# Kernel optimization log

Measured on AMD Instinct MI355X. Metric: run time of the kernel, lower is better.

The kernel has to match this reference:

```python
import jax, jax.numpy as jnp
import numpy as np

B, T, D_IN, D_FEAT, D_LAT = 256, 512, 128, 256, 512

def setup_inputs() -> dict:
    key = jax.random.key(0)
    ks = jax.random.split(key, 6)
    s = lambda fan_in: 1.0 / np.sqrt(fan_in)
    return {
        "x": jax.random.normal(ks[0], (B, T, D_IN), dtype=jnp.float32),
        "W_enc": jax.random.normal(ks[1], (D_IN, D_FEAT), dtype=jnp.float32) * s(D_IN),
        "b_enc": jnp.zeros((D_FEAT,), dtype=jnp.float32),
        "W_x": jax.random.normal(ks[2], (D_FEAT, 4 * D_LAT), dtype=jnp.float32) * s(D_FEAT),
        "W_h": jax.random.normal(ks[3], (D_LAT, 4 * D_LAT), dtype=jnp.float32) * s(D_LAT),
        "b_lstm": jnp.zeros((4 * D_LAT,), dtype=jnp.float32),
        "W_dec": jax.random.normal(ks[4], (D_LAT, 1), dtype=jnp.float32) * s(D_LAT),
        "b_dec": jnp.zeros((1,), dtype=jnp.float32),
    }

def reference(x, W_enc, b_enc, W_x, W_h, b_lstm, W_dec, b_dec):
    # Dense encoder with tanh: [B,T,D_IN] -> [B,T,D_FEAT]
    enc = jnp.tanh(jnp.einsum("bti,if->btf", x, W_enc) + b_enc)
    d = W_h.shape[0]
    # Precompute input-to-gate projection for all steps (hoisted out of loop)
    xz = jnp.einsum("btf,fg->btg", enc, W_x) + b_lstm  # [B,T,4d]
    xz_t = jnp.swapaxes(xz, 0, 1)  # [T,B,4d] for scan

    def step(carry, xz_step):
        h, c = carry
        z = xz_step + h @ W_h  # [B,4d]
        i, f, g, o = jnp.split(z, 4, axis=-1)  # Keras gate order: i,f,c,o
        i = jax.nn.sigmoid(i)
        f = jax.nn.sigmoid(f)
        g = jnp.tanh(g)
        o = jax.nn.sigmoid(o)
        c_new = f * c + i * g
        h_new = o * jnp.tanh(c_new)
        return (h_new, c_new), None

    h0 = jnp.zeros((x.shape[0], d), dtype=x.dtype)
    c0 = jnp.zeros((x.shape[0], d), dtype=x.dtype)
    (h_last, _), _ = jax.lax.scan(step, (h0, c0), xz_t)
    # Decoder on last hidden state: [B,d] -> [B,1]
    return h_last @ W_dec + b_dec
```

## Files before the change

### kernel.cpp

```cpp
#include <hip/hip_runtime.h>

#define BATCH 256
#define TLEN  512
#define DIN   128
#define DFEAT 256
#define DLAT  512
#define G4    2048
#define KCAT  768

typedef __bf16 bf16x8 __attribute__((ext_vector_type(8)));
typedef float f32x4 __attribute__((ext_vector_type(4)));

typedef __attribute__((address_space(1))) const unsigned int glb_u32;
typedef __attribute__((address_space(3))) unsigned int lds_u32;

#define WCAT_OFF   0u
#define WENC_OFF   3145728u
#define ENC_OFF    3211264u
#define H_OFF      70320128u
#define FLAG_OFF   70844416u

__device__ __forceinline__ float sigf(float x)  { return 1.0f / (1.0f + __expf(-x)); }
__device__ __forceinline__ float tanhfast(float x){ return 2.0f / (1.0f + __expf(-2.0f * x)) - 1.0f; }
__device__ __forceinline__ unsigned short bfb(float f) {
    __bf16 b = (__bf16)f;
    return __builtin_bit_cast(unsigned short, b);
}

__global__ __launch_bounds__(256) void wprep_kernel(const float* __restrict__ Wx,
                                                    const float* __restrict__ Wh,
                                                    const float* __restrict__ Wenc,
                                                    __bf16* __restrict__ wcat,
                                                    __bf16* __restrict__ wencf) {
    int cid = blockIdx.x * 256 + threadIdx.x;
    float v[8];
    __bf16* dst;
    if (cid < 196608) {
        int widx = cid / 12288;
        int r1 = cid % 12288;
        int nn = r1 / 1536;
        int r2 = r1 % 1536;
        int ks = r2 >> 6, l = r2 & 63;
        int col = (nn >> 1) * 512 + widx * 32 + (nn & 1) * 16 + (l & 15);
        int kc = ks * 32 + (l >> 4) * 8;
#pragma unroll
        for (int j = 0; j < 8; ++j) {
            int kk = kc + j;
            v[j] = (kk < DFEAT) ? Wx[kk * G4 + col] : Wh[(kk - DFEAT) * G4 + col];
        }
        dst = wcat + (size_t)cid * 8;
    } else {
        int c2 = cid - 196608;
        int ntg = c2 >> 8;
        int r = c2 & 255;
        int ks = r >> 6, l = r & 63;
        int col = ntg * 16 + (l & 15);
        int kc = ks * 32 + (l >> 4) * 8;
#pragma unroll
        for (int j = 0; j < 8; ++j) v[j] = Wenc[(kc + j) * DFEAT + col];
        dst = wencf + (size_t)c2 * 8;
    }
    bf16x8 o;
#pragma unroll
    for (int j = 0; j < 8; ++j) o[j] = (__bf16)v[j];
    *reinterpret_cast<bf16x8*>(dst) = o;
}

__global__ __launch_bounds__(256) void enc_kernel(const float* __restrict__ x,
                                                  const float* __restrict__ benc,
                                                  const __bf16* __restrict__ wencf,
                                                  __bf16* __restrict__ enc) {
    __shared__ uint4 afrag4[1024];
    __bf16* afrag = reinterpret_cast<__bf16*>(afrag4);
    int tid = threadIdx.x;
    int lane = tid & 63, w = tid >> 6;
    int rid0 = blockIdx.x * 64;
    int ntg0 = blockIdx.y * 4;

    bf16x8 wr[4][4];
#pragma unroll
    for (int n = 0; n < 4; ++n)
#pragma unroll
        for (int ks = 0; ks < 4; ++ks)
            wr[n][ks] = *reinterpret_cast<const bf16x8*>(
                wencf + (size_t)(((ntg0 + n) * 4 + ks) * 64 + lane) * 8);
    float bias[4];
#pragma unroll
    for (int n = 0; n < 4; ++n) bias[n] = benc[(ntg0 + n) * 16 + (lane & 15)];

#pragma unroll
    for (int i = 0; i < 4; ++i) {
        int c = tid + 256 * i;
        int row = c >> 4, k8 = c & 15;
        const float* src = x + (size_t)(rid0 + row) * DIN + k8 * 8;
        float4 f0 = *reinterpret_cast<const float4*>(src);
        float4 f1 = *reinterpret_cast<const float4*>(src + 4);
        bf16x8 o;
        o[0] = (__bf16)f0.x; o[1] = (__bf16)f0.y; o[2] = (__bf16)f0.z; o[3] = (__bf16)f0.w;
        o[4] = (__bf16)f1.x; o[5] = (__bf16)f1.y; o[6] = (__bf16)f1.z; o[7] = (__bf16)f1.w;
        int l = (k8 & 3) * 16 + (row & 15);
        int a16 = ((row >> 4) * 4 + (k8 >> 2)) * 64 + l;
        *reinterpret_cast<bf16x8*>(afrag + (size_t)a16 * 8) = o;
    }
    __syncthreads();

    int m = w;
    f32x4 acc[4];
#pragma unroll
    for (int n = 0; n < 4; ++n) acc[n] = (f32x4){bias[n], bias[n], bias[n], bias[n]};
#pragma unroll
    for (int ks = 0; ks < 4; ++ks) {
        bf16x8 a = *reinterpret_cast<const bf16x8*>(afrag + (size_t)((m * 4 + ks) * 64 + lane) * 8);
#pragma unroll
        for (int n = 0; n < 4; ++n)
            acc[n] = __builtin_amdgcn_mfma_f32_16x16x32_bf16(a, wr[n][ks], acc[n], 0, 0, 0);
    }
#pragma unroll
    for (int n = 0; n < 4; ++n) {
        int colg = (ntg0 + n) * 16 + (lane & 15);
#pragma unroll
        for (int q = 0; q < 4; ++q) {
            int rid = rid0 + m * 16 + (lane >> 4) * 4 + q;
            int bb = rid >> 9, tt = rid & 511;
            float th = tanhfast(acc[n][q]);
            enc[(size_t)(tt * BATCH + bb) * DFEAT + colg] = (__bf16)th;
        }
    }
}

__global__ __launch_bounds__(256, 1) void lstm_kernel(const __bf16* __restrict__ enc,
                                                      const __bf16* __restrict__ wcat,
                                                      const float* __restrict__ blstm,
                                                      __bf16* __restrict__ hbuf,
                                                      unsigned int* __restrict__ flags) {
    extern __shared__ char smem[];
    __bf16* afrag = reinterpret_cast<__bf16*>(smem);
    float* zbuf = reinterpret_cast<float*>(smem + 24576);

    const int tid = threadIdx.x;
    const int lane = tid & 63, np = tid >> 6;
    const int grp = blockIdx.x & 15, widx = blockIdx.x >> 4;
    const int b0 = grp * 16;

    bf16x8 wreg[2][24];
#pragma unroll
    for (int nt2 = 0; nt2 < 2; ++nt2)
#pragma unroll
        for (int ks = 0; ks < 24; ++ks)
            wreg[nt2][ks] = *reinterpret_cast<const bf16x8*>(
                wcat + (size_t)((((widx * 8 + np * 2 + nt2) * 24) + ks) * 64 + lane) * 8);
    const float bias0 = blstm[np * 512 + widx * 32 + (lane & 15)];
    const float bias1 = blstm[np * 512 + widx * 32 + 16 + (lane & 15)];

    const int row = tid & 15;
    const int kq = (tid >> 6) * 32 + ((tid >> 4) & 3) * 8;
    const __bf16* encp = enc + (size_t)(b0 + row) * DFEAT + kq;
    const __bf16* hpA = hbuf + (size_t)(b0 + row) * DLAT + kq;
    const __bf16* hpB = hpA + (size_t)BATCH * DLAT;
    __bf16* enc_lds = afrag + tid * 8;
    __bf16* h_lds = afrag + (512 + tid) * 8;
    const int cell = 2 * tid;
    const int crow = cell >> 5, ccol = cell & 31;
    unsigned* hdA = reinterpret_cast<unsigned*>(
        hbuf + (size_t)(b0 + crow) * DLAT + widx * 32 + ccol);
    unsigned* hdB = reinterpret_cast<unsigned*>(
        hbuf + (size_t)BATCH * DLAT + (size_t)(b0 + crow) * DLAT + widx * 32 + ccol);
    const unsigned* pollp = &flags[(grp * 16 + (lane >> 2)) * 16 + (lane & 3)];
    unsigned* myflag = &flags[(grp * 16 + widx) * 16 + np];
    const float* zg = zbuf + crow * 32 + ccol;
    float* zst = zbuf + np * 512 + ((lane >> 4) * 4) * 32 + (lane & 15);
    const __bf16* abase = afrag + lane * 8;

    float c0 = 0.f, c1 = 0.f;

    __builtin_amdgcn_global_load_lds((glb_u32*)encp, (lds_u32*)enc_lds, 16, 0, 0);
    __builtin_amdgcn_global_load_lds((glb_u32*)(encp + 128), (lds_u32*)(enc_lds + 2048), 16, 0, 0);
    encp += (size_t)BATCH * DFEAT;
    __syncthreads();

#pragma unroll 1
    for (int t = 0; t < TLEN; ++t) {
        f32x4 acc0 = (f32x4){bias0, bias0, bias0, bias0};
        f32x4 acc1 = (f32x4){bias1, bias1, bias1, bias1};
#pragma unroll
        for (int ks = 0; ks < 8; ++ks) {
            bf16x8 a = *reinterpret_cast<const bf16x8*>(abase + ks * 512);
            acc0 = __builtin_amdgcn_mfma_f32_16x16x32_bf16(a, wreg[0][ks], acc0, 0, 0, 0);
            acc1 = __builtin_amdgcn_mfma_f32_16x16x32_bf16(a, wreg[1][ks], acc1, 0, 0, 0);
        }

        if (t > 0) {
            unsigned v;
            do {
                v = __hip_atomic_load(pollp, __ATOMIC_RELAXED, __HIP_MEMORY_SCOPE_AGENT);
            } while (!__all((int)(v >= (unsigned)t)));

            const __bf16* hp = (t & 1) ? hpB : hpA;
            uint4 d0, d1, d2, d3;
            asm volatile(
                "global_load_dwordx4 %0, %4, off sc1\n\t"
                "global_load_dwordx4 %1, %4, off offset:256 sc1\n\t"
                "global_load_dwordx4 %2, %4, off offset:512 sc1\n\t"
                "global_load_dwordx4 %3, %4, off offset:768 sc1\n\t"
                "s_waitcnt vmcnt(0)"
                : "=&v"(d0), "=&v"(d1), "=&v"(d2), "=&v"(d3)
                : "v"(hp) : "memory");
            *reinterpret_cast<uint4*>(h_lds) = d0;
            *reinterpret_cast<uint4*>(h_lds + 2048) = d1;
            *reinterpret_cast<uint4*>(h_lds + 4096) = d2;
            *reinterpret_cast<uint4*>(h_lds + 6144) = d3;
            __syncthreads();

#pragma unroll
            for (int ks = 8; ks < 24; ++ks) {
                bf16x8 a = *reinterpret_cast<const bf16x8*>(abase + ks * 512);
                acc0 = __builtin_amdgcn_mfma_f32_16x16x32_bf16(a, wreg[0][ks], acc0, 0, 0, 0);
                acc1 = __builtin_amdgcn_mfma_f32_16x16x32_bf16(a, wreg[1][ks], acc1, 0, 0, 0);
            }
        }

#pragma unroll
        for (int q = 0; q < 4; ++q) {
            zst[q * 32] = acc0[q];
            zst[q * 32 + 16] = acc1[q];
        }
        __syncthreads();

        float2 zi = *reinterpret_cast<const float2*>(zg);
        float2 zf = *reinterpret_cast<const float2*>(zg + 512);
        float2 zgt = *reinterpret_cast<const float2*>(zg + 1024);
        float2 zo = *reinterpret_cast<const float2*>(zg + 1536);
        float i0 = sigf(zi.x), f0 = sigf(zf.x), g0 = tanhfast(zgt.x), o0 = sigf(zo.x);
        c0 = f0 * c0 + i0 * g0;
        float h0 = o0 * tanhfast(c0);
        float i1 = sigf(zi.y), f1 = sigf(zf.y), g1 = tanhfast(zgt.y), o1 = sigf(zo.y);
        c1 = f1 * c1 + i1 * g1;
        float h1 = o1 * tanhfast(c1);

        unsigned hpk = (unsigned)bfb(h0) | ((unsigned)bfb(h1) << 16);
        __hip_atomic_store(((t & 1) ? hdA : hdB), hpk, __ATOMIC_RELAXED,
                           __HIP_MEMORY_SCOPE_AGENT);

        asm volatile("s_waitcnt vmcnt(0)" ::: "memory");
        if (lane == 0)
            __hip_atomic_store(myflag, (unsigned)(t + 1), __ATOMIC_RELAXED,
                               __HIP_MEMORY_SCOPE_AGENT);

        if (t + 1 < TLEN) {
            __builtin_amdgcn_global_load_lds((glb_u32*)encp, (lds_u32*)enc_lds, 16, 0, 0);
            __builtin_amdgcn_global_load_lds((glb_u32*)(encp + 128),
                                             (lds_u32*)(enc_lds + 2048), 16, 0, 0);
            encp += (size_t)BATCH * DFEAT;
        }
        __syncthreads();
    }
}

__global__ __launch_bounds__(64) void dec_kernel(const __bf16* __restrict__ hbuf,
                                                 const float* __restrict__ wdec,
                                                 const float* __restrict__ bdec,
                                                 float* __restrict__ out) {
    int b = blockIdx.x, lane = threadIdx.x;
    uint4 d = *reinterpret_cast<const uint4*>(hbuf + (size_t)b * DLAT + lane * 8);
    const __bf16* hv = reinterpret_cast<const __bf16*>(&d);
    float4 w0 = *reinterpret_cast<const float4*>(wdec + lane * 8);
    float4 w1 = *reinterpret_cast<const float4*>(wdec + lane * 8 + 4);
    float s = (float)hv[0] * w0.x + (float)hv[1] * w0.y + (float)hv[2] * w0.z +
              (float)hv[3] * w0.w + (float)hv[4] * w1.x + (float)hv[5] * w1.y +
              (float)hv[6] * w1.z + (float)hv[7] * w1.w;
#pragma unroll
    for (int off = 32; off; off >>= 1) s += __shfl_xor(s, off);
    if (lane == 0) out[b] = s + bdec[0];
}

extern "C" void kernel_launch(void* const* d_in, const int* in_sizes, int n_in,
                              void* d_out, int out_size, void* d_ws, size_t ws_size,
                              hipStream_t stream) {
    (void)in_sizes; (void)n_in; (void)out_size; (void)ws_size;
    const float* x     = (const float*)d_in[0];
    const float* Wenc  = (const float*)d_in[1];
    const float* benc  = (const float*)d_in[2];
    const float* Wx    = (const float*)d_in[3];
    const float* Wh    = (const float*)d_in[4];
    const float* blstm = (const float*)d_in[5];
    const float* Wdec  = (const float*)d_in[6];
    const float* bdec  = (const float*)d_in[7];

    char* ws = (char*)d_ws;
    __bf16* wcat  = (__bf16*)(ws + WCAT_OFF);
    __bf16* wencf = (__bf16*)(ws + WENC_OFF);
    __bf16* enc   = (__bf16*)(ws + ENC_OFF);
    __bf16* hbuf  = (__bf16*)(ws + H_OFF);
    unsigned int* flags = (unsigned int*)(ws + FLAG_OFF);

    (void)hipMemsetAsync(ws + FLAG_OFF, 0, 16384, stream);

    wprep_kernel<<<784, 256, 0, stream>>>(Wx, Wh, Wenc, wcat, wencf);
    enc_kernel<<<dim3(2048, 4), 256, 0, stream>>>(x, benc, wencf, enc);

    (void)hipFuncSetAttribute(reinterpret_cast<const void*>(lstm_kernel),
                              hipFuncAttributeMaxDynamicSharedMemorySize, 90112);
    lstm_kernel<<<256, 256, 90112, stream>>>(enc, wcat, blstm, hbuf, flags);

    dec_kernel<<<256, 64, 0, stream>>>(hbuf, Wdec, bdec, (float*)d_out);
}
```

Baseline: 1.539 ms.

## Tag hidden-state words with step counter to replace flag polling

Each bf16 hidden value is now stored in a 32-bit word with a 16-bit step tag in the low half, so consumers poll the data itself until every tag matches the current step. This removes the separate flag array, the vmcnt wait before the flag store, and one round-trip of flag polling per step. The LSTM kernel also converts Wx/Wh to bf16 fragments directly from fp32 inside its prologue, which drops the weight-prep work for those matrices. In exchange the h exchange traffic doubles, and spinning on many data lines with s_sleep may add latency or memory contention.

```diff
diff --git a/kernel.cpp b/kernel.cpp
--- a/kernel.cpp
+++ b/kernel.cpp
@@ -14,11 +14,9 @@
 typedef __attribute__((address_space(1))) const unsigned int glb_u32;
 typedef __attribute__((address_space(3))) unsigned int lds_u32;
 
-#define WCAT_OFF   0u
-#define WENC_OFF   3145728u
-#define ENC_OFF    3211264u
-#define H_OFF      70320128u
-#define FLAG_OFF   70844416u
+#define WENC_OFF   0u
+#define ENC_OFF    65536u
+#define H_OFF      67174400u
 
 __device__ __forceinline__ float sigf(float x)  { return 1.0f / (1.0f + __expf(-x)); }
 __device__ __forceinline__ float tanhfast(float x){ return 2.0f / (1.0f + __expf(-2.0f * x)) - 1.0f; }
@@ -26,44 +24,22 @@
     __bf16 b = (__bf16)f;
     return __builtin_bit_cast(unsigned short, b);
 }
-
-__global__ __launch_bounds__(256) void wprep_kernel(const float* __restrict__ Wx,
-                                                    const float* __restrict__ Wh,
-                                                    const float* __restrict__ Wenc,
-                                                    __bf16* __restrict__ wcat,
+__device__ __forceinline__ float bfu(unsigned w) {
+    return (float)__builtin_bit_cast(__bf16, (unsigned short)(w >> 16));
+}
+
+__global__ __launch_bounds__(256) void wprep_kernel(const float* __restrict__ Wenc,
                                                     __bf16* __restrict__ wencf) {
-    int cid = blockIdx.x * 256 + threadIdx.x;
-    float v[8];
-    __bf16* dst;
-    if (cid < 196608) {
-        int widx = cid / 12288;
-        int r1 = cid % 12288;
-        int nn = r1 / 1536;
-        int r2 = r1 % 1536;
-        int ks = r2 >> 6, l = r2 & 63;
-        int col = (nn >> 1) * 512 + widx * 32 + (nn & 1) * 16 + (l & 15);
-        int kc = ks * 32 + (l >> 4) * 8;
-#pragma unroll
-        for (int j = 0; j < 8; ++j) {
-            int kk = kc + j;
-            v[j] = (kk < DFEAT) ? Wx[kk * G4 + col] : Wh[(kk - DFEAT) * G4 + col];
-        }
-        dst = wcat + (size_t)cid * 8;
-    } else {
-        int c2 = cid - 196608;
-        int ntg = c2 >> 8;
-        int r = c2 & 255;
-        int ks = r >> 6, l = r & 63;
-        int col = ntg * 16 + (l & 15);
-        int kc = ks * 32 + (l >> 4) * 8;
-#pragma unroll
-        for (int j = 0; j < 8; ++j) v[j] = Wenc[(kc + j) * DFEAT + col];
-        dst = wencf + (size_t)c2 * 8;
-    }
+    int c2 = blockIdx.x * 256 + threadIdx.x;
+    int ntg = c2 >> 8;
+    int r = c2 & 255;
+    int ks = r >> 6, l = r & 63;
+    int col = ntg * 16 + (l & 15);
+    int kc = ks * 32 + (l >> 4) * 8;
     bf16x8 o;
 #pragma unroll
-    for (int j = 0; j < 8; ++j) o[j] = (__bf16)v[j];
-    *reinterpret_cast<bf16x8*>(dst) = o;
+    for (int j = 0; j < 8; ++j) o[j] = (__bf16)Wenc[(kc + j) * DFEAT + col];
+    *reinterpret_cast<bf16x8*>(wencf + (size_t)c2 * 8) = o;
 }
 
 __global__ __launch_bounds__(256) void enc_kernel(const float* __restrict__ x,
@@ -129,10 +105,10 @@
 }
 
 __global__ __launch_bounds__(256, 1) void lstm_kernel(const __bf16* __restrict__ enc,
-                                                      const __bf16* __restrict__ wcat,
+                                                      const float* __restrict__ Wx,
+                                                      const float* __restrict__ Wh,
                                                       const float* __restrict__ blstm,
-                                                      __bf16* __restrict__ hbuf,
-                                                      unsigned int* __restrict__ flags) {
+                                                      unsigned* __restrict__ hbuf) {
     extern __shared__ char smem[];
     __bf16* afrag = reinterpret_cast<__bf16*>(smem);
     float* zbuf = reinterpret_cast<float*>(smem + 24576);
@@ -144,29 +120,38 @@
 
     bf16x8 wreg[2][24];
 #pragma unroll
-    for (int nt2 = 0; nt2 < 2; ++nt2)
-#pragma unroll
-        for (int ks = 0; ks < 24; ++ks)
-            wreg[nt2][ks] = *reinterpret_cast<const bf16x8*>(
-                wcat + (size_t)((((widx * 8 + np * 2 + nt2) * 24) + ks) * 64 + lane) * 8);
+    for (int nt2 = 0; nt2 < 2; ++nt2) {
+        const int col = np * 512 + widx * 32 + nt2 * 16 + (lane & 15);
+#pragma unroll
+        for (int ks = 0; ks < 24; ++ks) {
+            const int kb = ks * 32 + (lane >> 4) * 8;
+            bf16x8 f;
+#pragma unroll
+            for (int j = 0; j < 8; ++j) {
+                int kk = kb + j;
+                float w = (kk < DFEAT) ? Wx[(size_t)kk * G4 + col]
+                                       : Wh[(size_t)(kk - DFEAT) * G4 + col];
+                f[j] = (__bf16)w;
+            }
+            wreg[nt2][ks] = f;
+        }
+    }
     const float bias0 = blstm[np * 512 + widx * 32 + (lane & 15)];
     const float bias1 = blstm[np * 512 + widx * 32 + 16 + (lane & 15)];
 
     const int row = tid & 15;
     const int kq = (tid >> 6) * 32 + ((tid >> 4) & 3) * 8;
     const __bf16* encp = enc + (size_t)(b0 + row) * DFEAT + kq;
-    const __bf16* hpA = hbuf + (size_t)(b0 + row) * DLAT + kq;
-    const __bf16* hpB = hpA + (size_t)BATCH * DLAT;
+    const unsigned* hpA = hbuf + (size_t)(b0 + row) * DLAT + kq;
+    const unsigned* hpB = hpA + (size_t)BATCH * DLAT;
     __bf16* enc_lds = afrag + tid * 8;
     __bf16* h_lds = afrag + (512 + tid) * 8;
     const int cell = 2 * tid;
     const int crow = cell >> 5, ccol = cell & 31;
-    unsigned* hdA = reinterpret_cast<unsigned*>(
+    unsigned long long* hd0 = reinterpret_cast<unsigned long long*>(
         hbuf + (size_t)(b0 + crow) * DLAT + widx * 32 + ccol);
-    unsigned* hdB = reinterpret_cast<unsigned*>(
+    unsigned long long* hd1 = reinterpret_cast<unsigned long long*>(
         hbuf + (size_t)BATCH * DLAT + (size_t)(b0 + crow) * DLAT + widx * 32 + ccol);
-    const unsigned* pollp = &flags[(grp * 16 + (lane >> 2)) * 16 + (lane & 3)];
-    unsigned* myflag = &flags[(grp * 16 + widx) * 16 + np];
     const float* zg = zbuf + crow * 32 + ccol;
     float* zst = zbuf + np * 512 + ((lane >> 4) * 4) * 32 + (lane & 15);
     const __bf16* abase = afrag + lane * 8;
@@ -190,25 +175,30 @@
         }
 
         if (t > 0) {
-            unsigned v;
-            do {
-                v = __hip_atomic_load(pollp, __ATOMIC_RELAXED, __HIP_MEMORY_SCOPE_AGENT);
-            } while (!__all((int)(v >= (unsigned)t)));
-
-            const __bf16* hp = (t & 1) ? hpB : hpA;
-            uint4 d0, d1, d2, d3;
-            asm volatile(
-                "global_load_dwordx4 %0, %4, off sc1\n\t"
-                "global_load_dwordx4 %1, %4, off offset:256 sc1\n\t"
-                "global_load_dwordx4 %2, %4, off offset:512 sc1\n\t"
-                "global_load_dwordx4 %3, %4, off offset:768 sc1\n\t"
-                "s_waitcnt vmcnt(0)"
-                : "=&v"(d0), "=&v"(d1), "=&v"(d2), "=&v"(d3)
-                : "v"(hp) : "memory");
-            *reinterpret_cast<uint4*>(h_lds) = d0;
-            *reinterpret_cast<uint4*>(h_lds + 2048) = d1;
-            *reinterpret_cast<uint4*>(h_lds + 4096) = d2;
-            *reinterpret_cast<uint4*>(h_lds + 6144) = d3;
+            const unsigned tlo = (unsigned)t & 0xffffu;
+            const unsigned* hp = (t & 1) ? hpB : hpA;
+#pragma unroll
+            for (int ii = 0; ii < 4; ++ii) {
+                const unsigned* p = hp + ii * 128;
+                uint4 a, b;
+                for (;;) {
+                    asm volatile(
+                        "global_load_dwordx4 %0, %2, off sc1\n\t"
+                        "global_load_dwordx4 %1, %2, off offset:16 sc1\n\t"
+                        "s_waitcnt vmcnt(0)"
+                        : "=&v"(a), "=&v"(b) : "v"(p) : "memory");
+                    unsigned m = ((a.x ^ tlo) | (a.y ^ tlo) | (a.z ^ tlo) | (a.w ^ tlo) |
+                                  (b.x ^ tlo) | (b.y ^ tlo) | (b.z ^ tlo) | (b.w ^ tlo)) & 0xffffu;
+                    if (m == 0) break;
+                    __builtin_amdgcn_s_sleep(1);
+                }
+                uint4 o;
+                o.x = (a.x >> 16) | (a.y & 0xffff0000u);
+                o.y = (a.z >> 16) | (a.w & 0xffff0000u);
+                o.z = (b.x >> 16) | (b.y & 0xffff0000u);
+                o.w = (b.z >> 16) | (b.w & 0xffff0000u);
+                *reinterpret_cast<uint4*>(h_lds + ii * 2048) = o;
+            }
             __syncthreads();
 
 #pragma unroll
@@ -237,14 +227,12 @@
         c1 = f1 * c1 + i1 * g1;
         float h1 = o1 * tanhfast(c1);
 
-        unsigned hpk = (unsigned)bfb(h0) | ((unsigned)bfb(h1) << 16);
-        __hip_atomic_store(((t & 1) ? hdA : hdB), hpk, __ATOMIC_RELAXED,
+        const unsigned tago = (unsigned)(t + 1) & 0xffffu;
+        unsigned w0 = ((unsigned)bfb(h0) << 16) | tago;
+        unsigned w1 = ((unsigned)bfb(h1) << 16) | tago;
+        unsigned long long pk = (unsigned long long)w0 | ((unsigned long long)w1 << 32);
+        __hip_atomic_store(((t & 1) ? hd0 : hd1), pk, __ATOMIC_RELAXED,
                            __HIP_MEMORY_SCOPE_AGENT);
-
-        asm volatile("s_waitcnt vmcnt(0)" ::: "memory");
-        if (lane == 0)
-            __hip_atomic_store(myflag, (unsigned)(t + 1), __ATOMIC_RELAXED,
-                               __HIP_MEMORY_SCOPE_AGENT);
 
         if (t + 1 < TLEN) {
             __builtin_amdgcn_global_load_lds((glb_u32*)encp, (lds_u32*)enc_lds, 16, 0, 0);
@@ -256,18 +244,18 @@
     }
 }
 
-__global__ __launch_bounds__(64) void dec_kernel(const __bf16* __restrict__ hbuf,
+__global__ __launch_bounds__(64) void dec_kernel(const unsigned* __restrict__ hbuf,
                                                  const float* __restrict__ wdec,
                                                  const float* __restrict__ bdec,
                                                  float* __restrict__ out) {
     int b = blockIdx.x, lane = threadIdx.x;
-    uint4 d = *reinterpret_cast<const uint4*>(hbuf + (size_t)b * DLAT + lane * 8);
-    const __bf16* hv = reinterpret_cast<const __bf16*>(&d);
+    const unsigned* hrow = hbuf + (size_t)b * DLAT + lane * 8;
+    uint4 a = *reinterpret_cast<const uint4*>(hrow);
+    uint4 c = *reinterpret_cast<const uint4*>(hrow + 4);
     float4 w0 = *reinterpret_cast<const float4*>(wdec + lane * 8);
     float4 w1 = *reinterpret_cast<const float4*>(wdec + lane * 8 + 4);
-    float s = (float)hv[0] * w0.x + (float)hv[1] * w0.y + (float)hv[2] * w0.z +
-              (float)hv[3] * w0.w + (float)hv[4] * w1.x + (float)hv[5] * w1.y +
-              (float)hv[6] * w1.z + (float)hv[7] * w1.w;
+    float s = bfu(a.x) * w0.x + bfu(a.y) * w0.y + bfu(a.z) * w0.z + bfu(a.w) * w0.w +
+              bfu(c.x) * w1.x + bfu(c.y) * w1.y + bfu(c.z) * w1.z + bfu(c.w) * w1.w;
 #pragma unroll
     for (int off = 32; off; off >>= 1) s += __shfl_xor(s, off);
     if (lane == 0) out[b] = s + bdec[0];
@@ -287,20 +275,18 @@
     const float* bdec  = (const float*)d_in[7];
 
     char* ws = (char*)d_ws;
-    __bf16* wcat  = (__bf16*)(ws + WCAT_OFF);
     __bf16* wencf = (__bf16*)(ws + WENC_OFF);
     __bf16* enc   = (__bf16*)(ws + ENC_OFF);
-    __bf16* hbuf  = (__bf16*)(ws + H_OFF);
-    unsigned int* flags = (unsigned int*)(ws + FLAG_OFF);
-
-    (void)hipMemsetAsync(ws + FLAG_OFF, 0, 16384, stream);
-
-    wprep_kernel<<<784, 256, 0, stream>>>(Wx, Wh, Wenc, wcat, wencf);
+    unsigned* hbuf = (unsigned*)(ws + H_OFF);
+
+    (void)hipMemsetAsync(ws + H_OFF, 0, 1048576, stream);
+
+    wprep_kernel<<<16, 256, 0, stream>>>(Wenc, wencf);
     enc_kernel<<<dim3(2048, 4), 256, 0, stream>>>(x, benc, wencf, enc);
 
     (void)hipFuncSetAttribute(reinterpret_cast<const void*>(lstm_kernel),
                               hipFuncAttributeMaxDynamicSharedMemorySize, 90112);
-    lstm_kernel<<<256, 256, 90112, stream>>>(enc, wcat, blstm, hbuf, flags);
+    lstm_kernel<<<256, 256, 90112, stream>>>(enc, Wx, Wh, blstm, hbuf);
 
     dec_kernel<<<256, 64, 0, stream>>>(hbuf, Wdec, bdec, (float*)d_out);
 }
```

After: 1.885 ms. +22.5%, slower.
